# Kernel optimization log

Measured on AMD Instinct MI355X. Metric: run time of the kernel, lower is better.

Reference implementation:

```python
import jax, jax.numpy as jnp
import numpy as np

VOCAB, DIM, HEADS, LAYERS = 32000, 1024, 16, 2
B, S = 2, 1024
HD = DIM // HEADS


def rmsnorm(x, g, eps=1e-6):
    return x * jax.lax.rsqrt(jnp.mean(x * x, axis=-1, keepdims=True) + eps) * g


def setup_inputs() -> dict:
    key = jax.random.key(0)
    ks = jax.random.split(key, 20)
    s = 0.02
    d = {
        "text_ids": jax.random.randint(ks[0], (B, S), 0, VOCAB),
        "embed": jax.random.normal(ks[1], (VOCAB, DIM), jnp.float32) * s,
        "g1": jnp.ones((LAYERS, DIM), jnp.float32),
        "wq": jax.random.normal(ks[2], (LAYERS, DIM, DIM), jnp.float32) * s,
        "bq": jnp.zeros((LAYERS, DIM), jnp.float32),
        "wk": jax.random.normal(ks[3], (LAYERS, DIM, DIM), jnp.float32) * s,
        "bk": jnp.zeros((LAYERS, DIM), jnp.float32),
        "wv": jax.random.normal(ks[4], (LAYERS, DIM, DIM), jnp.float32) * s,
        "bv": jnp.zeros((LAYERS, DIM), jnp.float32),
        "wo": jax.random.normal(ks[5], (LAYERS, DIM, DIM), jnp.float32) * s,
        "bo": jnp.zeros((LAYERS, DIM), jnp.float32),
        "g2": jnp.ones((LAYERS, DIM), jnp.float32),
        "w1": jax.random.normal(ks[6], (LAYERS, DIM, 4 * DIM), jnp.float32) * s,
        "b1": jnp.zeros((LAYERS, 4 * DIM), jnp.float32),
        "w2": jax.random.normal(ks[7], (LAYERS, 4 * DIM, DIM), jnp.float32) * s,
        "b2": jnp.zeros((LAYERS, DIM), jnp.float32),
        "gf": jnp.ones((DIM,), jnp.float32),
        "head_w": jax.random.normal(ks[8], (DIM, VOCAB), jnp.float32) * s,
        "head_b": jnp.zeros((VOCAB,), jnp.float32),
    }
    return d


def reference(text_ids, embed, g1, wq, bq, wk, bk, wv, bv, wo, bo,
              g2, w1, b1, w2, b2, gf, head_w, head_b):
    b, s = text_ids.shape
    x = embed[text_ids]                                   # [B,S,D]
    causal = jnp.tril(jnp.ones((s, s), dtype=bool))        # [S,S]
    scale = 1.0 / jnp.sqrt(jnp.asarray(HD, x.dtype))
    for l in range(LAYERS):
        # attention sublayer: x = x + attn(norm1(x))
        h = rmsnorm(x, g1[l])
        q = (h @ wq[l] + bq[l]).reshape(b, s, HEADS, HD)
        k = (h @ wk[l] + bk[l]).reshape(b, s, HEADS, HD)
        v = (h @ wv[l] + bv[l]).reshape(b, s, HEADS, HD)
        scores = jnp.einsum("bqhd,bkhd->bhqk", q, k) * scale
        scores = jnp.where(causal, scores, jnp.asarray(-1e30, scores.dtype))
        a = jax.nn.softmax(scores, axis=-1)
        o = jnp.einsum("bhqk,bkhd->bqhd", a, v).reshape(b, s, DIM)
        x = x + (o @ wo[l] + bo[l])
        # FFN sublayer: x = x + ffn(norm2(x)), SiLU MLP (MoE unused in source forward)
        h2 = rmsnorm(x, g2[l])
        x = x + (jax.nn.silu(h2 @ w1[l] + b1[l]) @ w2[l] + b2[l])
    x = rmsnorm(x, gf)
    return x.astype(jnp.float32) @ head_w + head_b         # [B,S,VOCAB]
```

## Files before the change

### kernel.cpp

```cpp
#include <hip/hip_runtime.h>

#define LAYERS 2
#define DIM 1024
#define HEADS 16
#define HD 64
#define BATCH 2
#define SEQ 1024
#define ROWS (BATCH * SEQ)
#define FFN (4 * DIM)
#define VOCAB 32000
#define QKVN (3 * DIM)

typedef unsigned short u16;
typedef short vshort8 __attribute__((ext_vector_type(8)));
typedef float f32x4 __attribute__((ext_vector_type(4)));

#define VMCNT(n) asm volatile("s_waitcnt vmcnt(" #n ")" ::: "memory")

__device__ __forceinline__ u16 f2bf(float f) {
  union { float f; unsigned u; } x{f};
  unsigned r = (x.u + 0x7fffu + ((x.u >> 16) & 1u)) >> 16;
  return (u16)r;
}

__device__ __forceinline__ void gll16(const void* g, u16* l) {
  __builtin_amdgcn_global_load_lds(
      (const __attribute__((address_space(1))) void*)g,
      (__attribute__((address_space(3))) void*)l, 16, 0, 0);
}

__device__ __forceinline__ int xcd_swizzle(int orig, int nwg) {
  int q = nwg >> 3, r = nwg & 7;
  int xcd = orig & 7;
  int base = (xcd < r) ? xcd * (q + 1) : r * (q + 1) + (xcd - r) * q;
  return base + (orig >> 3);
}

__global__ __launch_bounds__(256) void transpose_sq_kernel(
    const float* __restrict__ wq, const float* __restrict__ wk,
    const float* __restrict__ wv, const float* __restrict__ wo,
    u16* __restrict__ wqkvT, u16* __restrict__ woT) {
  __shared__ float tile[32][33];
  int z = blockIdx.z, l = z >> 2, wsel = z & 3;
  const float* src =
      (wsel == 0 ? wq : wsel == 1 ? wk : wsel == 2 ? wv : wo) +
      (size_t)l * DIM * DIM;
  u16* dst = (wsel < 3)
                 ? wqkvT + (size_t)l * QKVN * DIM + (size_t)wsel * DIM * DIM
                 : woT + (size_t)l * DIM * DIM;
  int c0 = blockIdx.x * 32, r0 = blockIdx.y * 32;
  int tx = threadIdx.x, ty = threadIdx.y;
#pragma unroll
  for (int i = 0; i < 4; i++)
    tile[ty + i * 8][tx] = src[(size_t)(r0 + ty + i * 8) * DIM + c0 + tx];
  __syncthreads();
#pragma unroll
  for (int i = 0; i < 4; i++)
    dst[(size_t)(c0 + ty + i * 8) * DIM + r0 + tx] = f2bf(tile[tx][ty + i * 8]);
}

template <int R, int C>
__global__ __launch_bounds__(256) void transpose_rc_kernel(
    const float* __restrict__ srcb, u16* __restrict__ dstb) {
  __shared__ float tile[32][33];
  int l = blockIdx.z;
  const float* src = srcb + (size_t)l * R * C;
  u16* dst = dstb + (size_t)l * R * C;
  int c0 = blockIdx.x * 32, r0 = blockIdx.y * 32;
  int tx = threadIdx.x, ty = threadIdx.y;
#pragma unroll
  for (int i = 0; i < 4; i++)
    tile[ty + i * 8][tx] = src[(size_t)(r0 + ty + i * 8) * C + c0 + tx];
  __syncthreads();
#pragma unroll
  for (int i = 0; i < 4; i++)
    dst[(size_t)(c0 + ty + i * 8) * R + r0 + tx] = f2bf(tile[tx][ty + i * 8]);
}

__global__ __launch_bounds__(256) void pack_qkv_bias(
    const float* __restrict__ bq, const float* __restrict__ bk,
    const float* __restrict__ bv, float* __restrict__ o) {
  int l = blockIdx.y;
  int t = blockIdx.x * 256 + threadIdx.x;
  float v;
  if (t < DIM) v = bq[l * DIM + t];
  else if (t < 2 * DIM) v = bk[l * DIM + t - DIM];
  else v = bv[l * DIM + t - 2 * DIM];
  o[(size_t)l * QKVN + t] = v;
}

__global__ __launch_bounds__(256) void embed_norm_kernel(
    const int* __restrict__ ids, const float* __restrict__ emb,
    const float* __restrict__ g, float* __restrict__ x, u16* __restrict__ h) {
  int row = blockIdx.x;
  int t = threadIdx.x;
  int id = ids[row];
  float4 v = ((const float4*)(emb + (size_t)id * DIM))[t];
  ((float4*)(x + (size_t)row * DIM))[t] = v;
  float ss = v.x * v.x + v.y * v.y + v.z * v.z + v.w * v.w;
  for (int off = 32; off > 0; off >>= 1) ss += __shfl_down(ss, off);
  __shared__ float part[4];
  if ((t & 63) == 0) part[t >> 6] = ss;
  __syncthreads();
  float tot = part[0] + part[1] + part[2] + part[3];
  float r = rsqrtf(tot / (float)DIM + 1e-6f);
  float4 gv = ((const float4*)g)[t];
  ushort4 o;
  o.x = f2bf(v.x * r * gv.x);
  o.y = f2bf(v.y * r * gv.y);
  o.z = f2bf(v.z * r * gv.z);
  o.w = f2bf(v.w * r * gv.w);
  *(ushort4*)(h + (size_t)row * DIM + t * 4) = o;
}

__global__ __launch_bounds__(256) void addnorm_kernel(
    float* __restrict__ x, const float* __restrict__ P0,
    const float* __restrict__ P1, const float* __restrict__ bias,
    const float* __restrict__ g, u16* __restrict__ h) {
  int row = blockIdx.x;
  int t = threadIdx.x;
  float4 v = ((const float4*)(x + (size_t)row * DIM))[t];
  float4 a = ((const float4*)(P0 + (size_t)row * DIM))[t];
  float4 b = ((const float4*)(P1 + (size_t)row * DIM))[t];
  float4 c = ((const float4*)bias)[t];
  v.x += a.x + b.x + c.x;
  v.y += a.y + b.y + c.y;
  v.z += a.z + b.z + c.z;
  v.w += a.w + b.w + c.w;
  ((float4*)(x + (size_t)row * DIM))[t] = v;
  float ss = v.x * v.x + v.y * v.y + v.z * v.z + v.w * v.w;
  for (int off = 32; off > 0; off >>= 1) ss += __shfl_down(ss, off);
  __shared__ float part[4];
  if ((t & 63) == 0) part[t >> 6] = ss;
  __syncthreads();
  float tot = part[0] + part[1] + part[2] + part[3];
  float r = rsqrtf(tot / (float)DIM + 1e-6f);
  float4 gv = ((const float4*)g)[t];
  ushort4 o;
  o.x = f2bf(v.x * r * gv.x);
  o.y = f2bf(v.y * r * gv.y);
  o.z = f2bf(v.z * r * gv.z);
  o.w = f2bf(v.w * r * gv.w);
  *(ushort4*)(h + (size_t)row * DIM + t * 4) = o;
}

template <int OUTBF, int SILU, int SPLITK, int MFAST, int VT>
__global__ __launch_bounds__(256, 2) void gemm128_kernel(
    const u16* __restrict__ A, const u16* __restrict__ Wt,
    const float* __restrict__ bias, void* __restrict__ outv,
    float* __restrict__ pout1, u16* __restrict__ vt2, int M, int N, int K) {
  __shared__ u16 As[2][128 * 64];
  __shared__ u16 Bs[2][128 * 64];
  int nm = M >> 7, nn = N >> 7, nwg = nm * nn;
  int wg = xcd_swizzle(blockIdx.x, SPLITK ? nwg * 2 : nwg);
  int ks = 0;
  if (SPLITK) { ks = wg >= nwg; wg -= ks * nwg; }
  int mi, ni;
  if (MFAST) { mi = wg % nm; ni = wg / nm; }
  else       { ni = wg % nn; mi = wg / nn; }
  int m0 = mi << 7, n0 = ni << 7;
  int kb = SPLITK ? ks * (K >> 1) : 0;
  int NTt = (SPLITK ? (K >> 1) : K) >> 6;
  int tid = threadIdx.x, wave = tid >> 6, lane = tid & 63;
  int wr = wave >> 1, wc = wave & 1;
  int r16 = lane & 15, g4 = lane >> 4;
  int lrow = lane >> 3, lslot = lane & 7;

  f32x4 acc[4][4] = {};

  auto stage = [&](int buf, int kt) {
#pragma unroll
    for (int i = 0; i < 4; i++) {
      int s = wave * 4 + i;
      int row = s * 8 + lrow;
      int slot = lslot ^ (row & 7);
      gll16(A + (size_t)(m0 + row) * K + kb + kt * 64 + slot * 8,
            &As[buf][s * 512 + lane * 8]);
    }
#pragma unroll
    for (int i = 0; i < 4; i++) {
      int s = wave * 4 + i;
      int row = s * 8 + lrow;
      int slot = lslot ^ (row & 7);
      gll16(Wt + (size_t)(n0 + row) * K + kb + kt * 64 + slot * 8,
            &Bs[buf][s * 512 + lane * 8]);
    }
  };

  stage(0, 0);
  VMCNT(0);
  __builtin_amdgcn_s_barrier();

  for (int t = 0; t < NTt; t++) {
    int cur = t & 1;
    if (t + 1 < NTt) stage(cur ^ 1, t + 1);
#pragma unroll
    for (int kk = 0; kk < 2; kk++) {
      vshort8 af[4], bf[4];
#pragma unroll
      for (int m = 0; m < 4; m++) {
        int r = wr * 64 + m * 16 + r16;
        int slot = (kk * 4 + g4) ^ (r & 7);
        af[m] = *(const vshort8*)&As[cur][r * 64 + slot * 8];
      }
#pragma unroll
      for (int n = 0; n < 4; n++) {
        int c = wc * 64 + n * 16 + r16;
        int slot = (kk * 4 + g4) ^ (c & 7);
        bf[n] = *(const vshort8*)&Bs[cur][c * 64 + slot * 8];
      }
#pragma unroll
      for (int m = 0; m < 4; m++)
#pragma unroll
        for (int n = 0; n < 4; n++)
          acc[m][n] = __builtin_amdgcn_mfma_f32_16x16x32_bf16(af[m], bf[n],
                                                              acc[m][n], 0, 0, 0);
    }
    VMCNT(0);
    __builtin_amdgcn_s_barrier();
  }

  if (SPLITK) {
    float* P = ks ? pout1 : (float*)outv;
#pragma unroll
    for (int m = 0; m < 4; m++) {
      int rowb = m0 + wr * 64 + m * 16 + g4 * 4;
#pragma unroll
      for (int n = 0; n < 4; n++) {
        int col = n0 + wc * 64 + n * 16 + r16;
#pragma unroll
        for (int j = 0; j < 4; j++)
          P[(size_t)(rowb + j) * N + col] = acc[m][n][j];
      }
    }
  } else {
#pragma unroll
    for (int m = 0; m < 4; m++) {
      int rowb = m0 + wr * 64 + m * 16 + g4 * 4;
#pragma unroll
      for (int n = 0; n < 4; n++) {
        int col = n0 + wc * 64 + n * 16 + r16;
        float b = bias[col];
        u16 ov[4];
#pragma unroll
        for (int j = 0; j < 4; j++) {
          float v = acc[m][n][j] + b;
          if (SILU) v = v / (1.f + __expf(-v));
          if (OUTBF) ov[j] = f2bf(v);
          else ((float*)outv)[(size_t)(rowb + j) * N + col] = v;
        }
        if (OUTBF) {
          if (VT && col >= 2 * DIM) {
            int dv = col - 2 * DIM;
            int hh = dv >> 6, dd = dv & 63;
            int bb = rowb >> 10, s = rowb & 1023;
            ushort4 o4{ov[0], ov[1], ov[2], ov[3]};
            *(ushort4*)&vt2[((((size_t)(bb * 16 + hh) * (SEQ / 8) + (s >> 3)) * 64 +
                              dd) * 8) + (s & 7)] = o4;
          } else {
#pragma unroll
            for (int j = 0; j < 4; j++)
              ((u16*)outv)[(size_t)(rowb + j) * N + col] = ov[j];
          }
        }
      }
    }
  }
}

__global__ __launch_bounds__(512, 2) void gemm256p_kernel(
    const u16* __restrict__ A, const u16* __restrict__ Wt,
    const float* __restrict__ bias, float* __restrict__ out,
    int M, int N, int K) {
  __shared__ u16 As[2][256 * 64];
  __shared__ u16 Bs[2][256 * 64];
  int nn = N >> 8;
  int wg = xcd_swizzle(blockIdx.x, nn * 2);
  int ni = wg >> 1, mhalf = wg & 1;
  int n0 = ni << 8;
  int tid = threadIdx.x, w = tid >> 6, lane = tid & 63;
  int wr = w >> 2, wc = w & 3;
  int r16 = lane & 15, g4 = lane >> 4;
  int srow8 = lane >> 3, sslot = lane & 7;
  const int NTK = 16;
  const int NGT = 64;

  f32x4 acc[8][4] = {};

  auto stageA = [&](int buf, int mb, int kt, int hb, int j) {
    int chunk = j * 8 + w;
    int row = hb * 128 + chunk * 8 + srow8;
    int slot = sslot ^ (row & 7);
    gll16(A + (size_t)(mb + row) * K + kt * 64 + slot * 8,
          &As[buf][hb * 8192 + chunk * 512 + lane * 8]);
  };
  auto stageB = [&](int buf, int kt, int hb, int j) {
    int chunk = j * 8 + w;
    int row = hb * 128 + chunk * 8 + srow8;
    int slot = sslot ^ (row & 7);
    gll16(Wt + (size_t)(n0 + row) * K + kt * 64 + slot * 8,
          &Bs[buf][hb * 8192 + chunk * 512 + lane * 8]);
  };
  auto readA = [&](int buf, int mf, int kk) -> vshort8 {
    int row = mf * 32 + wr * 16 + r16;
    int slot = (kk * 4 + g4) ^ (row & 7);
    return *(const vshort8*)&As[buf][row * 64 + slot * 8];
  };
  auto readB = [&](int buf, int nf, int kk) -> vshort8 {
    int row = nf * 64 + wc * 16 + r16;
    int slot = (kk * 4 + g4) ^ (row & 7);
    return *(const vshort8*)&Bs[buf][row * 64 + slot * 8];
  };

  int mb0 = (mhalf * 4) << 8;
  stageA(0, mb0, 0, 0, 0); stageA(0, mb0, 0, 0, 1);
  stageB(0, 0, 0, 0);      stageB(0, 0, 0, 1);
  stageB(0, 0, 1, 0);      stageB(0, 0, 1, 1);
  stageA(0, mb0, 0, 1, 0); stageA(0, mb0, 0, 1, 1);
  VMCNT(0);
  __builtin_amdgcn_s_barrier();

  vshort8 af[4][2], bf0[2][2], bf1[2][2];

  for (int ti = 0; ti < 4; ti++) {
    int m0 = (mhalf * 4 + ti) << 8;
    for (int tt = 0; tt < NTK; tt++) {
      int gt = ti * NTK + tt;
      int cur = gt & 1, nxt = cur ^ 1;
      int gt1 = gt + 1;
      bool hn = gt1 < NGT;
      int kt1 = gt1 & (NTK - 1);
      int mb1 = (mhalf * 4 + (gt1 >> 4)) << 8;
#pragma unroll
      for (int m = 0; m < 4; m++)
#pragma unroll
        for (int kk = 0; kk < 2; kk++) af[m][kk] = readA(cur, m, kk);
#pragma unroll
      for (int n = 0; n < 2; n++)
#pragma unroll
        for (int kk = 0; kk < 2; kk++) bf0[n][kk] = readB(cur, n, kk);
      if (hn) { stageA(nxt, mb1, kt1, 0, 0); stageA(nxt, mb1, kt1, 0, 1); }
      __builtin_amdgcn_s_barrier();
      __builtin_amdgcn_s_setprio(1);
#pragma unroll
      for (int m = 0; m < 4; m++)
#pragma unroll
        for (int n = 0; n < 2; n++)
#pragma unroll
          for (int kk = 0; kk < 2; kk++)
            acc[m][n] = __builtin_amdgcn_mfma_f32_16x16x32_bf16(
                af[m][kk], bf0[n][kk], acc[m][n], 0, 0, 0);
      __builtin_amdgcn_s_setprio(0);
      VMCNT(4);
      __builtin_amdgcn_s_barrier();
#pragma unroll
      for (int n = 0; n < 2; n++)
#pragma unroll
        for (int kk = 0; kk < 2; kk++) bf1[n][kk] = readB(cur, 2 + n, kk);
      if (hn) { stageB(nxt, kt1, 0, 0); stageB(nxt, kt1, 0, 1); }
      __builtin_amdgcn_s_barrier();
      __builtin_amdgcn_s_setprio(1);
#pragma unroll
      for (int m = 0; m < 4; m++)
#pragma unroll
        for (int n = 0; n < 2; n++)
#pragma unroll
          for (int kk = 0; kk < 2; kk++)
            acc[m][n + 2] = __builtin_amdgcn_mfma_f32_16x16x32_bf16(
                af[m][kk], bf1[n][kk], acc[m][n + 2], 0, 0, 0);
      __builtin_amdgcn_s_setprio(0);
      VMCNT(4);
      __builtin_amdgcn_s_barrier();
#pragma unroll
      for (int m = 0; m < 4; m++)
#pragma unroll
        for (int kk = 0; kk < 2; kk++) af[m][kk] = readA(cur, 4 + m, kk);
      if (hn) { stageB(nxt, kt1, 1, 0); stageB(nxt, kt1, 1, 1); }
      __builtin_amdgcn_s_barrier();
      __builtin_amdgcn_s_setprio(1);
#pragma unroll
      for (int m = 0; m < 4; m++)
#pragma unroll
        for (int n = 0; n < 2; n++)
#pragma unroll
          for (int kk = 0; kk < 2; kk++)
            acc[m + 4][n + 2] = __builtin_amdgcn_mfma_f32_16x16x32_bf16(
                af[m][kk], bf1[n][kk], acc[m + 4][n + 2], 0, 0, 0);
      __builtin_amdgcn_s_setprio(0);
      VMCNT(4);
      __builtin_amdgcn_s_barrier();
      if (hn) { stageA(nxt, mb1, kt1, 1, 0); stageA(nxt, mb1, kt1, 1, 1); }
      __builtin_amdgcn_s_barrier();
      __builtin_amdgcn_s_setprio(1);
#pragma unroll
      for (int m = 0; m < 4; m++)
#pragma unroll
        for (int n = 0; n < 2; n++)
#pragma unroll
          for (int kk = 0; kk < 2; kk++)
            acc[m + 4][n] = __builtin_amdgcn_mfma_f32_16x16x32_bf16(
                af[m][kk], bf0[n][kk], acc[m + 4][n], 0, 0, 0);
      __builtin_amdgcn_s_setprio(0);
      VMCNT(4);
      __builtin_amdgcn_s_barrier();
    }
#pragma unroll
    for (int mf = 0; mf < 8; mf++) {
      int rowb = m0 + mf * 32 + wr * 16 + g4 * 4;
#pragma unroll
      for (int nf = 0; nf < 4; nf++) {
        int col = n0 + nf * 64 + wc * 16 + r16;
        float b = bias[col];
#pragma unroll
        for (int j = 0; j < 4; j++)
          out[(size_t)(rowb + j) * N + col] = acc[mf][nf][j] + b;
      }
    }
#pragma unroll
    for (int mf = 0; mf < 8; mf++)
#pragma unroll
      for (int nf = 0; nf < 4; nf++) acc[mf][nf] = f32x4{0.f, 0.f, 0.f, 0.f};
  }
}

__global__ __launch_bounds__(256) void attn_kernel(const u16* __restrict__ qkv,
                                                   const u16* __restrict__ vt2,
                                                   u16* __restrict__ o) {
  __shared__ u16 Ks[2][32 * 64];
  __shared__ u16 pl[4][16 * 40];
  int qblk = blockIdx.x, bh = blockIdx.y;
  int b = bh >> 4, h = bh & 15;
  int tid = threadIdx.x, w = tid >> 6, lane = tid & 63;
  int r16 = lane & 15, g4 = lane >> 4;
  int q0 = qblk * 64 + w * 16;

  const u16* qrow = qkv + ((size_t)(b * SEQ) + q0 + r16) * QKVN + h * HD;
  vshort8 aq0 = *(const vshort8*)(qrow + g4 * 8);
  vshort8 aq1 = *(const vshort8*)(qrow + 32 + g4 * 8);

  float mrun[4], lrun[4];
  f32x4 accO[4];
#pragma unroll
  for (int j = 0; j < 4; j++) { mrun[j] = -1e30f; lrun[j] = 0.f; }
#pragma unroll
  for (int d = 0; d < 4; d++) accO[d] = f32x4{0.f, 0.f, 0.f, 0.f};

  int nkvT = qblk * 2 + 2;
  auto stageK = [&](int buf, int kt) {
    int row = tid >> 3;
    int slot = (tid & 7) ^ (row & 7);
    gll16(qkv + ((size_t)(b * SEQ) + kt * 32 + row) * QKVN + DIM + h * HD + slot * 8,
          &Ks[buf][w * 512 + lane * 8]);
  };
  stageK(0, 0);
  __syncthreads();
  int buf = 0;
  for (int kt = 0; kt < nkvT; kt++) {
    int kv0 = kt * 32;
    if (kt + 1 < nkvT) stageK(buf ^ 1, kt + 1);
    if (kv0 <= q0 + 15) {
      int row0 = r16, row1 = 16 + r16;
      vshort8 bk00 = *(const vshort8*)&Ks[buf][row0 * 64 + ((0 + g4) ^ (row0 & 7)) * 8];
      vshort8 bk01 = *(const vshort8*)&Ks[buf][row0 * 64 + ((4 + g4) ^ (row0 & 7)) * 8];
      vshort8 bk10 = *(const vshort8*)&Ks[buf][row1 * 64 + ((0 + g4) ^ (row1 & 7)) * 8];
      vshort8 bk11 = *(const vshort8*)&Ks[buf][row1 * 64 + ((4 + g4) ^ (row1 & 7)) * 8];
      f32x4 s0 = {}, s1 = {};
      s0 = __builtin_amdgcn_mfma_f32_16x16x32_bf16(aq0, bk00, s0, 0, 0, 0);
      s0 = __builtin_amdgcn_mfma_f32_16x16x32_bf16(aq1, bk01, s0, 0, 0, 0);
      s1 = __builtin_amdgcn_mfma_f32_16x16x32_bf16(aq0, bk10, s1, 0, 0, 0);
      s1 = __builtin_amdgcn_mfma_f32_16x16x32_bf16(aq1, bk11, s1, 0, 0, 0);

#pragma unroll
      for (int j = 0; j < 4; j++) {
        int qg = q0 + g4 * 4 + j;
        float x0 = s0[j] * 0.125f;
        float x1 = s1[j] * 0.125f;
        if (kv0 + r16 > qg) x0 = -1e30f;
        if (kv0 + 16 + r16 > qg) x1 = -1e30f;
        float mx = fmaxf(x0, x1);
#pragma unroll
        for (int mm = 1; mm < 16; mm <<= 1) mx = fmaxf(mx, __shfl_xor(mx, mm));
        float mnew = fmaxf(mrun[j], mx);
        float alpha = __expf(mrun[j] - mnew);
        float p0 = __expf(x0 - mnew);
        float p1 = __expf(x1 - mnew);
        float rs = p0 + p1;
#pragma unroll
        for (int mm = 1; mm < 16; mm <<= 1) rs += __shfl_xor(rs, mm);
        lrun[j] = lrun[j] * alpha + rs;
        mrun[j] = mnew;
#pragma unroll
        for (int d = 0; d < 4; d++) accO[d][j] *= alpha;
        pl[w][(g4 * 4 + j) * 40 + r16] = f2bf(p0);
        pl[w][(g4 * 4 + j) * 40 + 16 + r16] = f2bf(p1);
      }
      asm volatile("s_waitcnt lgkmcnt(0)" ::: "memory");
      vshort8 ap = *(const vshort8*)&pl[w][r16 * 40 + g4 * 8];
      const u16* vbase = vt2 + (((size_t)bh * (SEQ / 8) + (kv0 >> 3) + g4) * 64) * 8;
#pragma unroll
      for (int d = 0; d < 4; d++) {
        vshort8 bv = *(const vshort8*)(vbase + (size_t)(d * 16 + r16) * 8);
        accO[d] = __builtin_amdgcn_mfma_f32_16x16x32_bf16(ap, bv, accO[d], 0, 0, 0);
      }
    }
    __syncthreads();
    buf ^= 1;
  }

#pragma unroll
  for (int j = 0; j < 4; j++) {
    float inv = 1.f / lrun[j];
    int row = q0 + g4 * 4 + j;
#pragma unroll
    for (int d = 0; d < 4; d++)
      o[((size_t)(b * SEQ) + row) * DIM + h * HD + d * 16 + r16] =
          f2bf(accO[d][j] * inv);
  }
}

extern "C" void kernel_launch(void* const* d_in, const int* in_sizes, int n_in,
                              void* d_out, int out_size, void* d_ws,
                              size_t ws_size, hipStream_t stream) {
  const int* ids = (const int*)d_in[0];
  const float* emb = (const float*)d_in[1];
  const float* g1 = (const float*)d_in[2];
  const float* wq = (const float*)d_in[3];
  const float* bq = (const float*)d_in[4];
  const float* wk = (const float*)d_in[5];
  const float* bk = (const float*)d_in[6];
  const float* wv = (const float*)d_in[7];
  const float* bv = (const float*)d_in[8];
  const float* wo = (const float*)d_in[9];
  const float* bo = (const float*)d_in[10];
  const float* g2 = (const float*)d_in[11];
  const float* w1 = (const float*)d_in[12];
  const float* b1 = (const float*)d_in[13];
  const float* w2 = (const float*)d_in[14];
  const float* b2 = (const float*)d_in[15];
  const float* gf = (const float*)d_in[16];
  const float* head_w = (const float*)d_in[17];
  const float* head_b = (const float*)d_in[18];
  float* out = (float*)d_out;

  char* ws = (char*)d_ws;
  size_t off = 0;
  auto alloc = [&](size_t bytes) -> char* {
    char* p = ws + off;
    off += (bytes + 255) & ~(size_t)255;
    return p;
  };
  u16* wqkvT = (u16*)alloc((size_t)LAYERS * QKVN * DIM * 2);
  u16* woT = (u16*)alloc((size_t)LAYERS * DIM * DIM * 2);
  u16* w1T = (u16*)alloc((size_t)LAYERS * DIM * FFN * 2);
  u16* w2T = (u16*)alloc((size_t)LAYERS * DIM * FFN * 2);
  u16* headT = (u16*)alloc((size_t)VOCAB * DIM * 2);
  float* bqkv = (float*)alloc((size_t)LAYERS * QKVN * 4);
  float* x = (float*)alloc((size_t)ROWS * DIM * 4);
  u16* h = (u16*)alloc((size_t)ROWS * DIM * 2);
  u16* qkvb = (u16*)alloc((size_t)ROWS * QKVN * 2);
  u16* vtb = (u16*)alloc((size_t)ROWS * DIM * 2);
  u16* ob = (u16*)alloc((size_t)ROWS * DIM * 2);
  u16* tb = (u16*)alloc((size_t)ROWS * FFN * 2);
  float* P0 = (float*)alloc((size_t)ROWS * DIM * 4);
  float* P1 = (float*)alloc((size_t)ROWS * DIM * 4);
  if (off > ws_size) return;

  dim3 tb32(32, 8);
  transpose_sq_kernel<<<dim3(DIM / 32, DIM / 32, 4 * LAYERS), tb32, 0, stream>>>(
      wq, wk, wv, wo, wqkvT, woT);
  transpose_rc_kernel<DIM, FFN>
      <<<dim3(FFN / 32, DIM / 32, LAYERS), tb32, 0, stream>>>(w1, w1T);
  transpose_rc_kernel<FFN, DIM>
      <<<dim3(DIM / 32, FFN / 32, LAYERS), tb32, 0, stream>>>(w2, w2T);
  transpose_rc_kernel<DIM, VOCAB>
      <<<dim3(VOCAB / 32, DIM / 32, 1), tb32, 0, stream>>>(head_w, headT);
  pack_qkv_bias<<<dim3(QKVN / 256, LAYERS), 256, 0, stream>>>(bq, bk, bv, bqkv);

  embed_norm_kernel<<<ROWS, 256, 0, stream>>>(ids, emb, g1, x, h);

  for (int l = 0; l < LAYERS; l++) {
    gemm128_kernel<1, 0, 0, 1, 1>
        <<<(ROWS / 128) * (QKVN / 128), 256, 0, stream>>>(
            h, wqkvT + (size_t)l * QKVN * DIM, bqkv + (size_t)l * QKVN,
            qkvb, nullptr, vtb, ROWS, QKVN, DIM);
    attn_kernel<<<dim3(SEQ / 64, BATCH * HEADS), 256, 0, stream>>>(qkvb, vtb, ob);
    gemm128_kernel<0, 0, 1, 0, 0>
        <<<2 * (ROWS / 128) * (DIM / 128), 256, 0, stream>>>(
            ob, woT + (size_t)l * DIM * DIM, nullptr, P0, P1, nullptr,
            ROWS, DIM, DIM);
    addnorm_kernel<<<ROWS, 256, 0, stream>>>(
        x, P0, P1, bo + (size_t)l * DIM, g2 + (size_t)l * DIM, h);
    gemm128_kernel<1, 1, 0, 1, 0>
        <<<(ROWS / 128) * (FFN / 128), 256, 0, stream>>>(
            h, w1T + (size_t)l * DIM * FFN, b1 + (size_t)l * FFN, tb, nullptr,
            nullptr, ROWS, FFN, DIM);
    gemm128_kernel<0, 0, 1, 0, 0>
        <<<2 * (ROWS / 128) * (DIM / 128), 256, 0, stream>>>(
            tb, w2T + (size_t)l * DIM * FFN, nullptr, P0, P1, nullptr,
            ROWS, DIM, FFN);
    addnorm_kernel<<<ROWS, 256, 0, stream>>>(
        x, P0, P1, b2 + (size_t)l * DIM,
        (l == LAYERS - 1) ? gf : (g1 + (size_t)(l + 1) * DIM), h);
  }
  gemm256p_kernel<<<(VOCAB / 256) * 2, 512, 0, stream>>>(
      h, headT, head_b, out, ROWS, VOCAB, DIM);
}
```

Measured before the change: 605.2 us.

## Vectorize weight transposes with 64x64 bf16 tiles and regroup GEMM prefetch stages

The weight transpose kernels now work on 64x64 tiles. They use float4 loads, convert to bf16 before writing to LDS, and emit 16-byte vectorized stores, so the one-time weight conversion uses fewer and wider memory transactions. The large GEMM's inner loop merges its prefetch stages into two batches and drops one barrier phase plus two vmcnt waits per K step, which cuts synchronization overhead. The relaxed waits (including VMCNT(4) in the prologue) risk reading LDS data that has not landed yet, if the outstanding-load counting is off.

After: 591.3 us. 1.02x faster.

```diff
diff --git a/kernel.cpp b/kernel.cpp
--- a/kernel.cpp
+++ b/kernel.cpp
@@ -36,11 +36,32 @@
   return base + (orig >> 3);
 }
 
+#define TRANS64_BODY(src, dst, C_, R_)                                        \
+  {                                                                           \
+    int lr = tid >> 4;                                                        \
+    int lc4 = (tid & 15) * 4;                                                 \
+    _Pragma("unroll") for (int i = 0; i < 4; i++) {                           \
+      int row = lr + i * 16;                                                  \
+      float4 v = *(const float4*)&src[(size_t)(r0 + row) * C_ + c0 + lc4];    \
+      ushort4 o{f2bf(v.x), f2bf(v.y), f2bf(v.z), f2bf(v.w)};                  \
+      *(ushort4*)&tl[row][lc4] = o;                                           \
+    }                                                                         \
+    __syncthreads();                                                          \
+    _Pragma("unroll") for (int i = 0; i < 2; i++) {                           \
+      int idx = tid + i * 256;                                                \
+      int ci = idx >> 3, ri0 = (idx & 7) * 8;                                 \
+      vshort8 o;                                                              \
+      _Pragma("unroll") for (int j = 0; j < 8; j++)                           \
+          o[j] = (short)tl[ri0 + j][ci];                                      \
+      *(vshort8*)&dst[(size_t)(c0 + ci) * R_ + r0 + ri0] = o;                 \
+    }                                                                         \
+  }
+
 __global__ __launch_bounds__(256) void transpose_sq_kernel(
     const float* __restrict__ wq, const float* __restrict__ wk,
     const float* __restrict__ wv, const float* __restrict__ wo,
     u16* __restrict__ wqkvT, u16* __restrict__ woT) {
-  __shared__ float tile[32][33];
+  __shared__ u16 tl[64][72];
   int z = blockIdx.z, l = z >> 2, wsel = z & 3;
   const float* src =
       (wsel == 0 ? wq : wsel == 1 ? wk : wsel == 2 ? wv : wo) +
@@ -48,33 +69,21 @@
   u16* dst = (wsel < 3)
                  ? wqkvT + (size_t)l * QKVN * DIM + (size_t)wsel * DIM * DIM
                  : woT + (size_t)l * DIM * DIM;
-  int c0 = blockIdx.x * 32, r0 = blockIdx.y * 32;
-  int tx = threadIdx.x, ty = threadIdx.y;
-#pragma unroll
-  for (int i = 0; i < 4; i++)
-    tile[ty + i * 8][tx] = src[(size_t)(r0 + ty + i * 8) * DIM + c0 + tx];
-  __syncthreads();
-#pragma unroll
-  for (int i = 0; i < 4; i++)
-    dst[(size_t)(c0 + ty + i * 8) * DIM + r0 + tx] = f2bf(tile[tx][ty + i * 8]);
+  int c0 = blockIdx.x * 64, r0 = blockIdx.y * 64;
+  int tid = threadIdx.x;
+  TRANS64_BODY(src, dst, DIM, DIM)
 }
 
 template <int R, int C>
 __global__ __launch_bounds__(256) void transpose_rc_kernel(
     const float* __restrict__ srcb, u16* __restrict__ dstb) {
-  __shared__ float tile[32][33];
+  __shared__ u16 tl[64][72];
   int l = blockIdx.z;
   const float* src = srcb + (size_t)l * R * C;
   u16* dst = dstb + (size_t)l * R * C;
-  int c0 = blockIdx.x * 32, r0 = blockIdx.y * 32;
-  int tx = threadIdx.x, ty = threadIdx.y;
-#pragma unroll
-  for (int i = 0; i < 4; i++)
-    tile[ty + i * 8][tx] = src[(size_t)(r0 + ty + i * 8) * C + c0 + tx];
-  __syncthreads();
-#pragma unroll
-  for (int i = 0; i < 4; i++)
-    dst[(size_t)(c0 + ty + i * 8) * R + r0 + tx] = f2bf(tile[tx][ty + i * 8]);
+  int c0 = blockIdx.x * 64, r0 = blockIdx.y * 64;
+  int tid = threadIdx.x;
+  TRANS64_BODY(src, dst, C, R)
 }
 
 __global__ __launch_bounds__(256) void pack_qkv_bias(
@@ -317,7 +326,7 @@
   stageB(0, 0, 0, 0);      stageB(0, 0, 0, 1);
   stageB(0, 0, 1, 0);      stageB(0, 0, 1, 1);
   stageA(0, mb0, 0, 1, 0); stageA(0, mb0, 0, 1, 1);
-  VMCNT(0);
+  VMCNT(4);
   __builtin_amdgcn_s_barrier();
 
   vshort8 af[4][2], bf0[2][2], bf1[2][2];
@@ -339,7 +348,10 @@
       for (int n = 0; n < 2; n++)
 #pragma unroll
         for (int kk = 0; kk < 2; kk++) bf0[n][kk] = readB(cur, n, kk);
-      if (hn) { stageA(nxt, mb1, kt1, 0, 0); stageA(nxt, mb1, kt1, 0, 1); }
+      if (hn) {
+        stageA(nxt, mb1, kt1, 0, 0); stageA(nxt, mb1, kt1, 0, 1);
+        stageB(nxt, kt1, 0, 0);      stageB(nxt, kt1, 0, 1);
+      }
       __builtin_amdgcn_s_barrier();
       __builtin_amdgcn_s_setprio(1);
 #pragma unroll
@@ -357,7 +369,6 @@
       for (int n = 0; n < 2; n++)
 #pragma unroll
         for (int kk = 0; kk < 2; kk++) bf1[n][kk] = readB(cur, 2 + n, kk);
-      if (hn) { stageB(nxt, kt1, 0, 0); stageB(nxt, kt1, 0, 1); }
       __builtin_amdgcn_s_barrier();
       __builtin_amdgcn_s_setprio(1);
 #pragma unroll
@@ -369,13 +380,15 @@
             acc[m][n + 2] = __builtin_amdgcn_mfma_f32_16x16x32_bf16(
                 af[m][kk], bf1[n][kk], acc[m][n + 2], 0, 0, 0);
       __builtin_amdgcn_s_setprio(0);
-      VMCNT(4);
       __builtin_amdgcn_s_barrier();
 #pragma unroll
       for (int m = 0; m < 4; m++)
 #pragma unroll
         for (int kk = 0; kk < 2; kk++) af[m][kk] = readA(cur, 4 + m, kk);
-      if (hn) { stageB(nxt, kt1, 1, 0); stageB(nxt, kt1, 1, 1); }
+      if (hn) {
+        stageB(nxt, kt1, 1, 0);      stageB(nxt, kt1, 1, 1);
+        stageA(nxt, mb1, kt1, 1, 0); stageA(nxt, mb1, kt1, 1, 1);
+      }
       __builtin_amdgcn_s_barrier();
       __builtin_amdgcn_s_setprio(1);
 #pragma unroll
@@ -386,12 +399,6 @@
           for (int kk = 0; kk < 2; kk++)
             acc[m + 4][n + 2] = __builtin_amdgcn_mfma_f32_16x16x32_bf16(
                 af[m][kk], bf1[n][kk], acc[m + 4][n + 2], 0, 0, 0);
-      __builtin_amdgcn_s_setprio(0);
-      VMCNT(4);
-      __builtin_amdgcn_s_barrier();
-      if (hn) { stageA(nxt, mb1, kt1, 1, 0); stageA(nxt, mb1, kt1, 1, 1); }
-      __builtin_amdgcn_s_barrier();
-      __builtin_amdgcn_s_setprio(1);
 #pragma unroll
       for (int m = 0; m < 4; m++)
 #pragma unroll
@@ -565,15 +572,15 @@
   float* P1 = (float*)alloc((size_t)ROWS * DIM * 4);
   if (off > ws_size) return;
 
-  dim3 tb32(32, 8);
-  transpose_sq_kernel<<<dim3(DIM / 32, DIM / 32, 4 * LAYERS), tb32, 0, stream>>>(
+  dim3 tb256(256);
+  transpose_sq_kernel<<<dim3(DIM / 64, DIM / 64, 4 * LAYERS), tb256, 0, stream>>>(
       wq, wk, wv, wo, wqkvT, woT);
   transpose_rc_kernel<DIM, FFN>
-      <<<dim3(FFN / 32, DIM / 32, LAYERS), tb32, 0, stream>>>(w1, w1T);
+      <<<dim3(FFN / 64, DIM / 64, LAYERS), tb256, 0, stream>>>(w1, w1T);
   transpose_rc_kernel<FFN, DIM>
-      <<<dim3(DIM / 32, FFN / 32, LAYERS), tb32, 0, stream>>>(w2, w2T);
+      <<<dim3(DIM / 64, FFN / 64, LAYERS), tb256, 0, stream>>>(w2, w2T);
   transpose_rc_kernel<DIM, VOCAB>
-      <<<dim3(VOCAB / 32, DIM / 32, 1), tb32, 0, stream>>>(head_w, headT);
+      <<<dim3(VOCAB / 64, DIM / 64, 1), tb256, 0, stream>>>(head_w, headT);
   pack_qkv_bias<<<dim3(QKVN / 256, LAYERS), 256, 0, stream>>>(bq, bk, bv, bqkv);
 
   embed_norm_kernel<<<ROWS, 256, 0, stream>>>(ids, emb, g1, x, h);
```
